# Kernel optimization log

Hardware: AMD Instinct MI355X
Metric: run time of the kernel (lower is better)

## Reference

```python
import jax, jax.numpy as jnp
import numpy as np
from jax import lax

B, N = 8, 4096
H = 128          # cfg.net.num_hidden
K = 64           # max_num_neighbors
R1, R2 = 0.2, 0.4
S1, S2 = N // 2, N // 8   # sampling ratios 0.5 and 0.25
OUT = 40


def setup_inputs() -> dict:
    key = jax.random.key(0)
    ks = jax.random.split(key, 32)
    inp = {}
    inp["x"] = jax.random.normal(ks[30], (B, N, 3), jnp.float32)
    inp["pos"] = jax.random.uniform(ks[31], (B, N, 3), jnp.float32)  # unit cube -> radii 0.2/0.4 meaningful
    layers = [("sa1_w1", "sa1_b1", 6, H // 2), ("sa1_w2", "sa1_b2", H // 2, H),
              ("sa2_w1", "sa2_b1", H + 3, H), ("sa2_w2", "sa2_b2", H, 2 * H),
              ("sa3_w1", "sa3_b1", 2 * H + 3, 2 * H), ("sa3_w2", "sa3_b2", 2 * H, 4 * H),
              ("sa3_w3", "sa3_b3", 4 * H, 8 * H),
              ("hd_w1", "hd_b1", 8 * H, 4 * H), ("hd_w2", "hd_b2", 4 * H, 2 * H),
              ("hd_w3", "hd_b3", 2 * H, OUT)]
    for i, (wn, bn, fi, fo) in enumerate(layers):
        inp[wn] = jax.random.normal(ks[i], (fi, fo), jnp.float32) / np.sqrt(fi)
        inp[bn] = jnp.zeros((fo,), jnp.float32)
    return inp


def _mlp(h, layers):
    # Linear+ReLU stack, plain last layer (PyG MLP plain_last=True, eval-mode BN is identity)
    n = len(layers)
    for i, (w, b) in enumerate(layers):
        h = h @ w + b
        if i < n - 1:
            h = jax.nn.relu(h)
    return h


def _fps(p, n_samples):
    # farthest point sampling on one cloud p: [N,3] -> [n_samples] int32
    Np = p.shape[0]

    def step(carry, _):
        min_d, last = carry
        d = jnp.sum((p - p[last]) ** 2, -1)
        min_d = jnp.minimum(min_d, d)
        return (min_d, jnp.argmax(min_d).astype(jnp.int32)), last

    _, idxs = lax.scan(step, (jnp.full((Np,), jnp.inf, p.dtype), jnp.int32(0)),
                       None, length=n_samples)
    return idxs


def _sa(xc, pc, n_samples, r, layers):
    # one SA layer on one cloud: xc [N,C], pc [N,3]
    idx = _fps(pc, n_samples)
    c = pc[idx]                                            # [S,3] centers
    d2 = jnp.sum((c[:, None, :] - pc[None, :, :]) ** 2, -1)  # [S,N]
    d2 = jnp.where(d2 <= r * r, d2, jnp.inf)               # ball query mask
    negd, nbr = lax.top_k(-d2, K)                          # K nearest inside ball
    valid = jnp.isfinite(negd)                             # [S,K]
    feat = jnp.concatenate([xc[nbr], pc[nbr] - c[:, None, :]], -1)  # [S,K,C+3]
    h = _mlp(feat, layers)                                 # [S,K,Cout]
    h = jnp.where(valid[..., None], h, -jnp.inf)
    return jnp.max(h, axis=1), c                           # max-pool over neighborhood


def reference(x, pos, sa1_w1, sa1_b1, sa1_w2, sa1_b2,
              sa2_w1, sa2_b1, sa2_w2, sa2_b2,
              sa3_w1, sa3_b1, sa3_w2, sa3_b2, sa3_w3, sa3_b3,
              hd_w1, hd_b1, hd_w2, hd_b2, hd_w3, hd_b3):
    x1, p1 = jax.vmap(lambda xc, pc: _sa(xc, pc, S1, R1,
                                         [(sa1_w1, sa1_b1), (sa1_w2, sa1_b2)]))(x, pos)
    x2, p2 = jax.vmap(lambda xc, pc: _sa(xc, pc, S2, R2,
                                         [(sa2_w1, sa2_b1), (sa2_w2, sa2_b2)]))(x1, p1)
    # GlobalSAModule: MLP(cat([x,pos])) then global max pool over remaining points
    g = _mlp(jnp.concatenate([x2, p2], -1),
             [(sa3_w1, sa3_b1), (sa3_w2, sa3_b2), (sa3_w3, sa3_b3)])
    g = jnp.max(g, axis=1)                                 # [B, 8H]
    # head MLP (dropout inactive at eval)
    return _mlp(g, [(hd_w1, hd_b1), (hd_w2, hd_b2), (hd_w3, hd_b3)])
```

## Files before the change

kernel.cpp:

```cpp
#include <hip/hip_runtime.h>


constexpr int NBATCH = 8;

template<int CTRL>
__device__ __forceinline__ float dpp_max_step(float v) {
  int o = __builtin_amdgcn_update_dpp(__float_as_int(v), __float_as_int(v),
                                      CTRL, 0xf, 0xf, false);
  return fmaxf(v, __int_as_float(o));
}
__device__ __forceinline__ float wave_max_bcast(float v) {
  v = dpp_max_step<0x111>(v);
  v = dpp_max_step<0x112>(v);
  v = dpp_max_step<0x114>(v);
  v = dpp_max_step<0x118>(v);
  v = dpp_max_step<0x142>(v);
  v = dpp_max_step<0x143>(v);
  return __int_as_float(__builtin_amdgcn_readlane(__float_as_int(v), 63));
}
template<int CTRL>
__device__ __forceinline__ int dpp_add_step(int v) {
  int o = __builtin_amdgcn_update_dpp(0, v, CTRL, 0xf, 0xf, true);
  return v + o;
}
__device__ __forceinline__ int wave_sum_bcast(int v) {
  v = dpp_add_step<0x111>(v);
  v = dpp_add_step<0x112>(v);
  v = dpp_add_step<0x114>(v);
  v = dpp_add_step<0x118>(v);
  v = dpp_add_step<0x142>(v);
  v = dpp_add_step<0x143>(v);
  return __builtin_amdgcn_readlane(v, 63);
}

__device__ void fps1_one(const float* __restrict__ p, float* __restrict__ cb) {
#pragma clang fp contract(off)
  constexpr int NTH = 256, PT = 16, NW = 4, NSAMP = 2048;
  __shared__ unsigned long long skey[2][NW];
  __shared__ float sxyz[2][NW][3];
  __shared__ float scb[NSAMP * 3];
  const int t = threadIdx.x, lane = t & 63, w = t >> 6;
  const float INF = __builtin_inff();
  float px[PT], py[PT], pz[PT], md[PT];
#pragma unroll
  for (int i = 0; i < PT; i++) {
    int j = t * PT + i;
    px[i] = p[j * 3 + 0]; py[i] = p[j * 3 + 1]; pz[i] = p[j * 3 + 2];
    md[i] = INF;
  }
  float cx = p[0], cy = p[1], cz = p[2];
  if (t == 0) { scb[0] = cx; scb[1] = cy; scb[2] = cz; }
  for (int s = 0; s < NSAMP - 1; ++s) {
#pragma unroll
    for (int i = 0; i < PT; i++) {
      float dx = px[i] - cx, dy = py[i] - cy, dz = pz[i] - cz;
      float d = (dx * dx + dy * dy) + dz * dz;
      md[i] = fminf(md[i], d);
    }
    float m8[8];
#pragma unroll
    for (int i = 0; i < 8; i++) m8[i] = fmaxf(md[i], md[i + 8]);
    float m4[4];
#pragma unroll
    for (int i = 0; i < 4; i++) m4[i] = fmaxf(m8[i], m8[i + 4]);
    float bv = fmaxf(fmaxf(m4[0], m4[1]), fmaxf(m4[2], m4[3]));
    int bi = 0;
#pragma unroll
    for (int i = PT - 1; i >= 1; --i) if (md[i] == bv) bi = i;
    float wmax = wave_max_bcast(bv);
    unsigned long long ball = __ballot(bv == wmax);
    int fl = __ffsll((long long)ball) - 1;
    int ib = __builtin_amdgcn_readlane(bi, fl);
    int gidx = ((w << 6) + fl) * PT + ib;
    float sx = px[0], sy = py[0], sz = pz[0];
#pragma unroll
    for (int k = 1; k < PT; k++)
      if (ib == k) { sx = px[k]; sy = py[k]; sz = pz[k]; }
    sx = __int_as_float(__builtin_amdgcn_readlane(__float_as_int(sx), fl));
    sy = __int_as_float(__builtin_amdgcn_readlane(__float_as_int(sy), fl));
    sz = __int_as_float(__builtin_amdgcn_readlane(__float_as_int(sz), fl));
    if (lane == 0) {
      skey[s & 1][w] = (((unsigned long long)(unsigned)__float_as_int(wmax)) << 32)
                       | (unsigned)(~gidx);
      sxyz[s & 1][w][0] = sx; sxyz[s & 1][w][1] = sy; sxyz[s & 1][w][2] = sz;
    }
    __syncthreads();
    unsigned long long best = skey[s & 1][0];
    float nx = sxyz[s & 1][0][0], ny = sxyz[s & 1][0][1], nz = sxyz[s & 1][0][2];
#pragma unroll
    for (int q = 1; q < NW; q++) {
      unsigned long long k2 = skey[s & 1][q];
      bool gt = k2 > best;
      best = gt ? k2 : best;
      nx = gt ? sxyz[s & 1][q][0] : nx;
      ny = gt ? sxyz[s & 1][q][1] : ny;
      nz = gt ? sxyz[s & 1][q][2] : nz;
    }
    cx = nx; cy = ny; cz = nz;
    if (t == 0) { scb[(s + 1) * 3 + 0] = cx; scb[(s + 1) * 3 + 1] = cy;
                  scb[(s + 1) * 3 + 2] = cz; }
  }
  __syncthreads();
  for (int i = t; i < NSAMP * 3; i += NTH) cb[i] = scb[i];
}

__device__ void fps2_one(const float* __restrict__ p, float* __restrict__ cb) {
#pragma clang fp contract(off)
  constexpr int NTH = 256, PT = 8, NW = 4, NSAMP = 512;
  __shared__ unsigned long long skey2[2][NW];
  __shared__ float sxyz2[2][NW][3];
  __shared__ float scb2[NSAMP * 3];
  const int t = threadIdx.x, lane = t & 63, w = t >> 6;
  const float INF = __builtin_inff();
  float px[PT], py[PT], pz[PT], md[PT];
#pragma unroll
  for (int i = 0; i < PT; i++) {
    int j = t * PT + i;
    px[i] = p[j * 3 + 0]; py[i] = p[j * 3 + 1]; pz[i] = p[j * 3 + 2];
    md[i] = INF;
  }
  float cx = p[0], cy = p[1], cz = p[2];
  if (t == 0) { scb2[0] = cx; scb2[1] = cy; scb2[2] = cz; }
  for (int s = 0; s < NSAMP - 1; ++s) {
#pragma unroll
    for (int i = 0; i < PT; i++) {
      float dx = px[i] - cx, dy = py[i] - cy, dz = pz[i] - cz;
      float d = (dx * dx + dy * dy) + dz * dz;
      md[i] = fminf(md[i], d);
    }
    float m4[4];
#pragma unroll
    for (int i = 0; i < 4; i++) m4[i] = fmaxf(md[i], md[i + 4]);
    float bv = fmaxf(fmaxf(m4[0], m4[1]), fmaxf(m4[2], m4[3]));
    int bi = 0;
#pragma unroll
    for (int i = PT - 1; i >= 1; --i) if (md[i] == bv) bi = i;
    float wmax = wave_max_bcast(bv);
    unsigned long long ball = __ballot(bv == wmax);
    int fl = __ffsll((long long)ball) - 1;
    int ib = __builtin_amdgcn_readlane(bi, fl);
    int gidx = ((w << 6) + fl) * PT + ib;
    float sx = px[0], sy = py[0], sz = pz[0];
#pragma unroll
    for (int k = 1; k < PT; k++)
      if (ib == k) { sx = px[k]; sy = py[k]; sz = pz[k]; }
    sx = __int_as_float(__builtin_amdgcn_readlane(__float_as_int(sx), fl));
    sy = __int_as_float(__builtin_amdgcn_readlane(__float_as_int(sy), fl));
    sz = __int_as_float(__builtin_amdgcn_readlane(__float_as_int(sz), fl));
    if (lane == 0) {
      skey2[s & 1][w] = (((unsigned long long)(unsigned)__float_as_int(wmax)) << 32)
                        | (unsigned)(~gidx);
      sxyz2[s & 1][w][0] = sx; sxyz2[s & 1][w][1] = sy; sxyz2[s & 1][w][2] = sz;
    }
    __syncthreads();
    unsigned long long best = skey2[s & 1][0];
    float nx = sxyz2[s & 1][0][0], ny = sxyz2[s & 1][0][1], nz = sxyz2[s & 1][0][2];
#pragma unroll
    for (int q = 1; q < NW; q++) {
      unsigned long long k2 = skey2[s & 1][q];
      bool gt = k2 > best;
      best = gt ? k2 : best;
      nx = gt ? sxyz2[s & 1][q][0] : nx;
      ny = gt ? sxyz2[s & 1][q][1] : ny;
      nz = gt ? sxyz2[s & 1][q][2] : nz;
    }
    cx = nx; cy = ny; cz = nz;
    if (t == 0) { scb2[(s + 1) * 3 + 0] = cx; scb2[(s + 1) * 3 + 1] = cy;
                  scb2[(s + 1) * 3 + 2] = cz; }
  }
  __syncthreads();
  for (int i = t; i < NSAMP * 3; i += NTH) cb[i] = scb2[i];
}

template<int NPTS, int SPB, int LCAP, int WPB>
__device__ void ballquery_body(int bb, const float* __restrict__ pts,
    const float* __restrict__ ctr, float rr,
    int* __restrict__ nbr, int* __restrict__ cnt_out) {
#pragma clang fp contract(off)
  constexpr int KREG = LCAP / 64;
  const int gw = bb * WPB + (threadIdx.x >> 6);
  const int lane = threadIdx.x & 63;
  const int b = gw / SPB;
  __shared__ unsigned long long list_[WPB][LCAP];
  unsigned long long* list = list_[threadIdx.x >> 6];
  const float* p = pts + (size_t)b * NPTS * 3;
  const float* c = ctr + (size_t)gw * 3;
  const float cx = c[0], cy = c[1], cz = c[2];
  const unsigned long long lmask = (1ull << lane) - 1ull;
  int cnt = 0;
  for (int j0 = 0; j0 < NPTS; j0 += 64) {
    int j = j0 + lane;
    float dx = p[j * 3 + 0] - cx, dy = p[j * 3 + 1] - cy, dz = p[j * 3 + 2] - cz;
    float d = (dx * dx + dy * dy) + dz * dz;
    bool in = (d <= rr);
    unsigned long long bal = __ballot(in);
    int pos = cnt + __popcll(bal & lmask);
    if (in && pos < LCAP)
      list[pos] = (((unsigned long long)__float_as_uint(d)) << 32) | (unsigned)j;
    cnt += __popcll(bal);
  }
  if (cnt > LCAP) cnt = LCAP;
  __syncthreads();
  int* nbrp = nbr + (size_t)gw * 64;
  const int nr = (cnt + 63) >> 6;
  unsigned long long key[KREG];
#pragma unroll
  for (int r = 0; r < KREG; r++) {
    int slot = r * 64 + lane;
    key[r] = (r < nr && slot < cnt) ? list[slot] : ~0ull;
  }
  if (cnt <= 64) {
    nbrp[lane] = (lane < cnt) ? (int)(unsigned)key[0] : 0;
    if (lane == 0) cnt_out[gw] = cnt;
    return;
  }
  unsigned pref = 0; int cbase = 0;
  for (int bit = 29; bit >= 0; --bit) {
    int cc = 0;
#pragma unroll
    for (int r = 0; r < KREG; r++) if (r < nr) {
      unsigned db = (unsigned)(key[r] >> 32);
      cc += ((db >> bit) == (pref >> bit)) ? 1 : 0;
    }
    cc = wave_sum_bcast(cc);
    if (cbase + cc < 64) { cbase += cc; pref |= (1u << bit); }
  }
  int base = 0;
#pragma unroll
  for (int r = 0; r < KREG; r++) if (r < nr) {
    unsigned db = (unsigned)(key[r] >> 32);
    bool sel = db < pref;
    unsigned long long m = __ballot(sel);
    if (sel) nbrp[base + __popcll(m & lmask)] = (int)(unsigned)key[r];
    base += __popcll(m);
  }
  int need = 64 - base;
  for (int t2 = 0; t2 < need; ++t2) {
    unsigned besti = 0xffffffffu;
#pragma unroll
    for (int r = 0; r < KREG; r++) if (r < nr) {
      if ((unsigned)(key[r] >> 32) == pref) {
        unsigned v = (unsigned)key[r];
        besti = v < besti ? v : besti;
      }
    }
#pragma unroll
    for (int off = 32; off; off >>= 1) {
      unsigned o = __shfl_xor(besti, off, 64);
      besti = o < besti ? o : besti;
    }
    unsigned long long wk = (((unsigned long long)pref) << 32) | besti;
#pragma unroll
    for (int r = 0; r < KREG; r++) if (r < nr && key[r] == wk) key[r] = ~0ull;
    if (lane == 0) nbrp[base + t2] = (int)besti;
  }
  if (lane == 0) cnt_out[gw] = 64;
}

__device__ void q1_body(int bb, const float* __restrict__ x,
    const float* __restrict__ pos, const float* __restrict__ w, float* __restrict__ q) {
  int gw = (bb << 2) + (threadIdx.x >> 6), lane = threadIdx.x & 63;
  const float* xr = x + (size_t)gw * 3; const float* pr = pos + (size_t)gw * 3;
  float a = 0.f;
#pragma unroll
  for (int m = 0; m < 3; m++) a = fmaf(xr[m], w[m * 64 + lane], a);
#pragma unroll
  for (int m = 0; m < 3; m++) a = fmaf(pr[m], w[(3 + m) * 64 + lane], a);
  q[(size_t)gw * 64 + lane] = a;
}

__device__ void t1_body(int bb, const float* __restrict__ c1,
    const float* __restrict__ w, const float* __restrict__ b1, float* __restrict__ t) {
  int gw = (bb << 2) + (threadIdx.x >> 6), lane = threadIdx.x & 63;
  const float* cr = c1 + (size_t)gw * 3;
  float a = b1[lane];
#pragma unroll
  for (int m = 0; m < 3; m++) a = fmaf(-cr[m], w[(3 + m) * 64 + lane], a);
  t[(size_t)gw * 64 + lane] = a;
}

__device__ void t2_body(int bb, const float* __restrict__ c2,
    const float* __restrict__ w, const float* __restrict__ b1, float* __restrict__ t) {
  int gw = (bb << 2) + (threadIdx.x >> 6), lane = threadIdx.x & 63;
  const float* cr = c2 + (size_t)gw * 3;
  float a0 = b1[lane], a1 = b1[64 + lane];
#pragma unroll
  for (int m = 0; m < 3; m++) {
    a0 = fmaf(-cr[m], w[(128 + m) * 128 + lane], a0);
    a1 = fmaf(-cr[m], w[(128 + m) * 128 + 64 + lane], a1);
  }
  t[(size_t)gw * 128 + lane] = a0;
  t[(size_t)gw * 128 + 64 + lane] = a1;
}

__device__ void concat3_body(int bb, const float* __restrict__ c2, float* __restrict__ xin3) {
  int row = bb * 256 + threadIdx.x;
  if (row < NBATCH * 512) {
    float* o = xin3 + (size_t)row * 272 + 256;
    const float* c = c2 + (size_t)row * 3;
    o[0] = c[0]; o[1] = c[1]; o[2] = c[2];
#pragma unroll
    for (int i = 3; i < 16; i++) o[i] = 0.f;
  }
}

template<int CIN, int COUT, int OSTR, int NPB, int SPB>
__device__ void sa_pool_body(int bb, const float* __restrict__ q,
    const float* __restrict__ t, const int* __restrict__ nbr, const int* __restrict__ cnt,
    const float* __restrict__ w2, const float* __restrict__ b2, float* __restrict__ out) {
  int gw = (bb << 2) + (threadIdx.x >> 6), lane = threadIdx.x & 63;
  int b = gw / SPB;
  int nk = nbr[(size_t)gw * 64 + lane];
  int c = cnt[gw];
  const float* qr = q + ((size_t)b * NPB + nk) * CIN;
  const float* tr = t + (size_t)gw * CIN;
  float h[CIN];
#pragma unroll
  for (int i = 0; i < CIN; i += 4) {
    float4 v = *(const float4*)(qr + i);
    h[i]     = fmaxf(v.x + tr[i], 0.f);
    h[i + 1] = fmaxf(v.y + tr[i + 1], 0.f);
    h[i + 2] = fmaxf(v.z + tr[i + 2], 0.f);
    h[i + 3] = fmaxf(v.w + tr[i + 3], 0.f);
  }
  bool valid = lane < c;
  float* op = out + (size_t)gw * OSTR;
#pragma unroll 1
  for (int nc = 0; nc < COUT; nc += 16) {
    float acc[16];
#pragma unroll
    for (int u = 0; u < 16; u++) acc[u] = b2[nc + u];
#pragma unroll
    for (int i = 0; i < CIN; i++) {
      const float* wr = w2 + (size_t)i * COUT + nc;
#pragma unroll
      for (int u = 0; u < 16; u++) acc[u] = fmaf(h[i], wr[u], acc[u]);
    }
#pragma unroll
    for (int u = 0; u < 16; u++) {
      float v = valid ? acc[u] : -__builtin_inff();
#pragma unroll
      for (int off = 32; off; off >>= 1) v = fmaxf(v, __shfl_xor(v, off, 64));
      acc[u] = v;
    }
    if (lane == 0) {
#pragma unroll
      for (int u = 0; u < 16; u += 4)
        *(float4*)(op + nc + u) = make_float4(acc[u], acc[u + 1], acc[u + 2], acc[u + 3]);
    }
  }
}

__global__ __attribute__((amdgpu_flat_work_group_size(256, 256),
                          amdgpu_waves_per_eu(1, 2)))
void fuse1_kernel(const float* __restrict__ pos,
    const float* __restrict__ x, const float* __restrict__ w11,
    float* __restrict__ c1, float* __restrict__ q1) {
  int bid = blockIdx.x;
  if (bid < 8)
    fps1_one(pos + (size_t)bid * 4096 * 3, c1 + (size_t)bid * 2048 * 3);
  else
    q1_body(bid - 8, x, pos, w11, q1);
}

__global__ __attribute__((amdgpu_flat_work_group_size(256, 256),
                          amdgpu_waves_per_eu(1, 2)))
void fuse2_kernel(const float* __restrict__ pos,
    const float* __restrict__ c1, const float* __restrict__ w11, const float* __restrict__ b11,
    float* __restrict__ c2, int* __restrict__ nbr1, int* __restrict__ cnt1,
    float* __restrict__ t1buf, float rr1) {
  int bid = blockIdx.x;
  if (bid < 8)
    fps2_one(c1 + (size_t)bid * 2048 * 3, c2 + (size_t)bid * 512 * 3);
  else if (bid < 8 + 4096)
    ballquery_body<4096, 2048, 512, 4>(bid - 8, pos, c1, rr1, nbr1, cnt1);
  else
    t1_body(bid - (8 + 4096), c1, w11, b11, t1buf);
}

__global__ __launch_bounds__(256) void fuse3_kernel(const float* __restrict__ q1buf,
    const float* __restrict__ t1buf, const int* __restrict__ nbr1, const int* __restrict__ cnt1,
    const float* __restrict__ w12, const float* __restrict__ b12, float* __restrict__ x1,
    const float* __restrict__ c1, const float* __restrict__ c2, float rr2,
    int* __restrict__ nbr2, int* __restrict__ cnt2,
    const float* __restrict__ w21, const float* __restrict__ b21, float* __restrict__ t2buf,
    float* __restrict__ xin3) {
  int bid = blockIdx.x;
  if (bid < 4096)
    sa_pool_body<64, 128, 128, 4096, 2048>(bid, q1buf, t1buf, nbr1, cnt1, w12, b12, x1);
  else if (bid < 4096 + 1024)
    ballquery_body<2048, 512, 1024, 4>(bid - 4096, c1, c2, rr2, nbr2, cnt2);
  else if (bid < 4096 + 1024 + 1024)
    t2_body(bid - (4096 + 1024), c2, w21, b21, t2buf);
  else
    concat3_body(bid - (4096 + 1024 + 1024), c2, xin3);
}

__global__ __launch_bounds__(256) void q2_kernel(const float* __restrict__ x1,
    const float* __restrict__ p1, const float* __restrict__ w, float* __restrict__ q2) {
  int gw = (blockIdx.x << 2) + (threadIdx.x >> 6), lane = threadIdx.x & 63;
  const float* xr = x1 + (size_t)gw * 128; const float* pr = p1 + (size_t)gw * 3;
  float a0 = 0.f, a1 = 0.f;
#pragma unroll 8
  for (int m = 0; m < 128; m++) {
    float v = xr[m];
    a0 = fmaf(v, w[m * 128 + lane], a0);
    a1 = fmaf(v, w[m * 128 + 64 + lane], a1);
  }
#pragma unroll
  for (int m = 0; m < 3; m++) {
    float v = pr[m];
    a0 = fmaf(v, w[(128 + m) * 128 + lane], a0);
    a1 = fmaf(v, w[(128 + m) * 128 + 64 + lane], a1);
  }
  q2[(size_t)gw * 128 + lane] = a0;
  q2[(size_t)gw * 128 + 64 + lane] = a1;
}

__global__ __launch_bounds__(256) void sa_pool2_kernel(const float* __restrict__ q,
    const float* __restrict__ t, const int* __restrict__ nbr, const int* __restrict__ cnt,
    const float* __restrict__ w2, const float* __restrict__ b2, float* __restrict__ out) {
  sa_pool_body<128, 256, 272, 2048, 512>(blockIdx.x, q, t, nbr, cnt, w2, b2, out);
}

template<int K, int KP, int N, int AST, bool RELU>
__global__ __launch_bounds__(256) void gemm64(const float* __restrict__ A,
    const float* __restrict__ W, const float* __restrict__ bias, float* __restrict__ C) {
  constexpr int NT = N / 64;
  const int bid = blockIdx.x, tid = threadIdx.x;
  const int tm = bid / NT, tn = bid % NT;
  __shared__ __align__(16) float As[16][68];
  __shared__ __align__(16) float Ws[16][68];
  const int arow = tid >> 2, acol = (tid & 3) << 2;
  const int wrow = tid >> 4, wcol = (tid & 15) << 2;
  const int ty = tid >> 4, tx = tid & 15;
  const float* Ap = A + (size_t)(tm * 64 + arow) * AST + acol;
  const float* Wp = W + (size_t)tn * 64 + wcol;
  float acc[4][4] = {};
  for (int k0 = 0; k0 < KP; k0 += 16) {
    float4 av = *(const float4*)(Ap + k0);
    As[acol + 0][arow] = av.x; As[acol + 1][arow] = av.y;
    As[acol + 2][arow] = av.z; As[acol + 3][arow] = av.w;
    int krow = k0 + wrow;
    float4 wv = make_float4(0.f, 0.f, 0.f, 0.f);
    if (krow < K) wv = *(const float4*)(Wp + (size_t)krow * N);
    *(float4*)(&Ws[wrow][wcol]) = wv;
    __syncthreads();
#pragma unroll
    for (int kk = 0; kk < 16; kk++) {
      float4 a4 = *(const float4*)(&As[kk][ty << 2]);
      float4 b4 = *(const float4*)(&Ws[kk][tx << 2]);
      float aa[4] = {a4.x, a4.y, a4.z, a4.w};
      float bb[4] = {b4.x, b4.y, b4.z, b4.w};
#pragma unroll
      for (int mm = 0; mm < 4; mm++)
#pragma unroll
        for (int nn = 0; nn < 4; nn++) acc[mm][nn] = fmaf(aa[mm], bb[nn], acc[mm][nn]);
    }
    __syncthreads();
  }
  const int m0 = tm * 64 + (ty << 2), n0 = tn * 64 + (tx << 2);
#pragma unroll
  for (int mm = 0; mm < 4; mm++) {
    float4 o;
    o.x = acc[mm][0] + bias[n0 + 0];
    o.y = acc[mm][1] + bias[n0 + 1];
    o.z = acc[mm][2] + bias[n0 + 2];
    o.w = acc[mm][3] + bias[n0 + 3];
    if (RELU) { o.x = fmaxf(o.x, 0.f); o.y = fmaxf(o.y, 0.f);
                o.z = fmaxf(o.z, 0.f); o.w = fmaxf(o.w, 0.f); }
    *(float4*)(C + (size_t)(m0 + mm) * N + n0) = o;
  }
}

__global__ void gmax_kernel(const float* __restrict__ h, float* __restrict__ g) {
  int n = blockIdx.x * 256 + threadIdx.x;
  int b = n >> 10, col = n & 1023;
  const float* p = h + ((size_t)b * 512) * 1024 + col;
  float m = -__builtin_inff();
  for (int j = 0; j < 512; j++) m = fmaxf(m, p[(size_t)j * 1024]);
  g[n] = m;
}

__global__ __launch_bounds__(256) void head_kernel(const float* __restrict__ g,
    const float* __restrict__ w1, const float* __restrict__ b1,
    const float* __restrict__ w2, const float* __restrict__ b2,
    const float* __restrict__ w3, const float* __restrict__ b3,
    float* __restrict__ out) {
  int b = blockIdx.x, t = threadIdx.x;
  __shared__ float s1[1024];
  __shared__ float s2[512];
  *(float4*)(s1 + t * 4) = *(const float4*)(g + (size_t)b * 1024 + t * 4);
  __syncthreads();
  {
    float a0 = b1[t], a1 = b1[t + 256];
    for (int i = 0; i < 1024; i++) {
      float v = s1[i];
      a0 = fmaf(v, w1[(size_t)i * 512 + t], a0);
      a1 = fmaf(v, w1[(size_t)i * 512 + t + 256], a1);
    }
    s2[t] = fmaxf(a0, 0.f); s2[t + 256] = fmaxf(a1, 0.f);
  }
  __syncthreads();
  {
    float a = b2[t];
    for (int i = 0; i < 512; i++) a = fmaf(s2[i], w2[(size_t)i * 256 + t], a);
    s1[t] = fmaxf(a, 0.f);
  }
  __syncthreads();
  if (t < 40) {
    float a = b3[t];
    for (int i = 0; i < 256; i++) a = fmaf(s1[i], w3[(size_t)i * 40 + t], a);
    out[(size_t)b * 40 + t] = a;
  }
}

extern "C" void kernel_launch(void* const* d_in, const int* in_sizes, int n_in,
                              void* d_out, int out_size, void* d_ws, size_t ws_size,
                              hipStream_t stream) {
  const float* x   = (const float*)d_in[0];
  const float* pos = (const float*)d_in[1];
  const float* w11 = (const float*)d_in[2];  const float* b11 = (const float*)d_in[3];
  const float* w12 = (const float*)d_in[4];  const float* b12 = (const float*)d_in[5];
  const float* w21 = (const float*)d_in[6];  const float* b21 = (const float*)d_in[7];
  const float* w22 = (const float*)d_in[8];  const float* b22 = (const float*)d_in[9];
  const float* w31 = (const float*)d_in[10]; const float* b31 = (const float*)d_in[11];
  const float* w32 = (const float*)d_in[12]; const float* b32 = (const float*)d_in[13];
  const float* w33 = (const float*)d_in[14]; const float* b33 = (const float*)d_in[15];
  const float* hw1 = (const float*)d_in[16]; const float* hb1 = (const float*)d_in[17];
  const float* hw2 = (const float*)d_in[18]; const float* hb2 = (const float*)d_in[19];
  const float* hw3 = (const float*)d_in[20]; const float* hb3 = (const float*)d_in[21];
  float* out = (float*)d_out;

  char* wsb = (char*)d_ws;
  int*   cnt1 = (int*)(wsb + 81920);
  int*   cnt2 = (int*)(wsb + 147456);
  float* c1   = (float*)(wsb + 163840);
  float* c2   = (float*)(wsb + 360448);
  float* g    = (float*)(wsb + 409600);
  char* big = wsb + 524288;
  int*   nbr1 = (int*)(big + 0);
  float* q1   = (float*)(big + 4194304);
  float* t1   = (float*)(big + 12582912);
  float* h3c  = (float*)(big + 0);
  float* x1   = (float*)(big + 16777216);
  int*   nbr2 = (int*)(big + 25165824);
  float* h3b  = (float*)(big + 16777216);
  float* q2   = (float*)(big + 26214400);
  float* h3a  = (float*)(big + 26214400);
  float* t2   = (float*)(big + 34603008);
  float* xin3 = (float*)(big + 36700160);

  const float RR1 = (float)(0.2 * 0.2);
  const float RR2 = (float)(0.4 * 0.4);

  fuse1_kernel<<<8 + 8192, 256, 0, stream>>>(pos, x, w11, c1, q1);
  fuse2_kernel<<<8 + 4096 + 4096, 256, 0, stream>>>(pos, c1, w11, b11,
                                                    c2, nbr1, cnt1, t1, RR1);
  fuse3_kernel<<<4096 + 1024 + 1024 + 16, 256, 0, stream>>>(q1, t1, nbr1, cnt1,
      w12, b12, x1, c1, c2, RR2, nbr2, cnt2, w21, b21, t2, xin3);
  q2_kernel<<<4096, 256, 0, stream>>>(x1, c1, w21, q2);
  sa_pool2_kernel<<<1024, 256, 0, stream>>>(q2, t2, nbr2, cnt2, w22, b22, xin3);
  gemm64<259, 272, 256, 272, true ><<<256,  256, 0, stream>>>(xin3, w31, b31, h3a);
  gemm64<256, 256, 512, 256, true ><<<512,  256, 0, stream>>>(h3a,  w32, b32, h3b);
  gemm64<512, 512, 1024, 512, false><<<1024, 256, 0, stream>>>(h3b, w33, b33, h3c);
  gmax_kernel<<<32, 256, 0, stream>>>(h3c, g);
  head_kernel<<<NBATCH, 256, 0, stream>>>(g, hw1, hb1, hw2, hb2, hw3, hb3, out);

  (void)in_sizes; (void)n_in; (void)out_size; (void)ws_size;
}
```

Baseline: 3.616 ms.

## Reschedule fused stages so FPS2 overlaps SA1 pooling instead of ball query

```diff
diff --git a/kernel.cpp b/kernel.cpp
--- a/kernel.cpp
+++ b/kernel.cpp
@@ -293,6 +293,27 @@
   t[(size_t)gw * 128 + 64 + lane] = a1;
 }
 
+__device__ void q2_body(int bb, const float* __restrict__ x1,
+    const float* __restrict__ p1, const float* __restrict__ w, float* __restrict__ q2) {
+  int gw = (bb << 2) + (threadIdx.x >> 6), lane = threadIdx.x & 63;
+  const float* xr = x1 + (size_t)gw * 128; const float* pr = p1 + (size_t)gw * 3;
+  float a0 = 0.f, a1 = 0.f;
+#pragma unroll 8
+  for (int m = 0; m < 128; m++) {
+    float v = xr[m];
+    a0 = fmaf(v, w[m * 128 + lane], a0);
+    a1 = fmaf(v, w[m * 128 + 64 + lane], a1);
+  }
+#pragma unroll
+  for (int m = 0; m < 3; m++) {
+    float v = pr[m];
+    a0 = fmaf(v, w[(128 + m) * 128 + lane], a0);
+    a1 = fmaf(v, w[(128 + m) * 128 + 64 + lane], a1);
+  }
+  q2[(size_t)gw * 128 + lane] = a0;
+  q2[(size_t)gw * 128 + 64 + lane] = a1;
+}
+
 __device__ void concat3_body(int bb, const float* __restrict__ c2, float* __restrict__ xin3) {
   int row = bb * 256 + threadIdx.x;
   if (row < NBATCH * 512) {
@@ -363,58 +384,42 @@
     q1_body(bid - 8, x, pos, w11, q1);
 }
 
-__global__ __attribute__((amdgpu_flat_work_group_size(256, 256),
-                          amdgpu_waves_per_eu(1, 2)))
-void fuse2_kernel(const float* __restrict__ pos,
+__global__ __launch_bounds__(256) void stage2_kernel(const float* __restrict__ pos,
     const float* __restrict__ c1, const float* __restrict__ w11, const float* __restrict__ b11,
-    float* __restrict__ c2, int* __restrict__ nbr1, int* __restrict__ cnt1,
-    float* __restrict__ t1buf, float rr1) {
+    int* __restrict__ nbr1, int* __restrict__ cnt1, float* __restrict__ t1buf, float rr1) {
+  int bid = blockIdx.x;
+  if (bid < 4096)
+    ballquery_body<4096, 2048, 512, 4>(bid, pos, c1, rr1, nbr1, cnt1);
+  else
+    t1_body(bid - 4096, c1, w11, b11, t1buf);
+}
+
+__global__ __launch_bounds__(256) void stage3_kernel(const float* __restrict__ c1,
+    float* __restrict__ c2,
+    const float* __restrict__ q1buf, const float* __restrict__ t1buf,
+    const int* __restrict__ nbr1, const int* __restrict__ cnt1,
+    const float* __restrict__ w12, const float* __restrict__ b12, float* __restrict__ x1) {
   int bid = blockIdx.x;
   if (bid < 8)
     fps2_one(c1 + (size_t)bid * 2048 * 3, c2 + (size_t)bid * 512 * 3);
-  else if (bid < 8 + 4096)
-    ballquery_body<4096, 2048, 512, 4>(bid - 8, pos, c1, rr1, nbr1, cnt1);
   else
-    t1_body(bid - (8 + 4096), c1, w11, b11, t1buf);
-}
-
-__global__ __launch_bounds__(256) void fuse3_kernel(const float* __restrict__ q1buf,
-    const float* __restrict__ t1buf, const int* __restrict__ nbr1, const int* __restrict__ cnt1,
-    const float* __restrict__ w12, const float* __restrict__ b12, float* __restrict__ x1,
-    const float* __restrict__ c1, const float* __restrict__ c2, float rr2,
+    sa_pool_body<64, 128, 128, 4096, 2048>(bid - 8, q1buf, t1buf, nbr1, cnt1, w12, b12, x1);
+}
+
+__global__ __launch_bounds__(256) void stage4_kernel(const float* __restrict__ c1,
+    const float* __restrict__ c2, float rr2,
     int* __restrict__ nbr2, int* __restrict__ cnt2,
     const float* __restrict__ w21, const float* __restrict__ b21, float* __restrict__ t2buf,
-    float* __restrict__ xin3) {
+    const float* __restrict__ x1, float* __restrict__ q2buf, float* __restrict__ xin3) {
   int bid = blockIdx.x;
-  if (bid < 4096)
-    sa_pool_body<64, 128, 128, 4096, 2048>(bid, q1buf, t1buf, nbr1, cnt1, w12, b12, x1);
-  else if (bid < 4096 + 1024)
-    ballquery_body<2048, 512, 1024, 4>(bid - 4096, c1, c2, rr2, nbr2, cnt2);
-  else if (bid < 4096 + 1024 + 1024)
-    t2_body(bid - (4096 + 1024), c2, w21, b21, t2buf);
+  if (bid < 1024)
+    ballquery_body<2048, 512, 1024, 4>(bid, c1, c2, rr2, nbr2, cnt2);
+  else if (bid < 1024 + 1024)
+    t2_body(bid - 1024, c2, w21, b21, t2buf);
+  else if (bid < 1024 + 1024 + 4096)
+    q2_body(bid - 2048, x1, c1, w21, q2buf);
   else
-    concat3_body(bid - (4096 + 1024 + 1024), c2, xin3);
-}
-
-__global__ __launch_bounds__(256) void q2_kernel(const float* __restrict__ x1,
-    const float* __restrict__ p1, const float* __restrict__ w, float* __restrict__ q2) {
-  int gw = (blockIdx.x << 2) + (threadIdx.x >> 6), lane = threadIdx.x & 63;
-  const float* xr = x1 + (size_t)gw * 128; const float* pr = p1 + (size_t)gw * 3;
-  float a0 = 0.f, a1 = 0.f;
-#pragma unroll 8
-  for (int m = 0; m < 128; m++) {
-    float v = xr[m];
-    a0 = fmaf(v, w[m * 128 + lane], a0);
-    a1 = fmaf(v, w[m * 128 + 64 + lane], a1);
-  }
-#pragma unroll
-  for (int m = 0; m < 3; m++) {
-    float v = pr[m];
-    a0 = fmaf(v, w[(128 + m) * 128 + lane], a0);
-    a1 = fmaf(v, w[(128 + m) * 128 + 64 + lane], a1);
-  }
-  q2[(size_t)gw * 128 + lane] = a0;
-  q2[(size_t)gw * 128 + 64 + lane] = a1;
+    concat3_body(bid - (1024 + 1024 + 4096), c2, xin3);
 }
 
 __global__ __launch_bounds__(256) void sa_pool2_kernel(const float* __restrict__ q,
@@ -555,11 +560,12 @@
   const float RR2 = (float)(0.4 * 0.4);
 
   fuse1_kernel<<<8 + 8192, 256, 0, stream>>>(pos, x, w11, c1, q1);
-  fuse2_kernel<<<8 + 4096 + 4096, 256, 0, stream>>>(pos, c1, w11, b11,
-                                                    c2, nbr1, cnt1, t1, RR1);
-  fuse3_kernel<<<4096 + 1024 + 1024 + 16, 256, 0, stream>>>(q1, t1, nbr1, cnt1,
-      w12, b12, x1, c1, c2, RR2, nbr2, cnt2, w21, b21, t2, xin3);
-  q2_kernel<<<4096, 256, 0, stream>>>(x1, c1, w21, q2);
+  stage2_kernel<<<4096 + 4096, 256, 0, stream>>>(pos, c1, w11, b11,
+                                                 nbr1, cnt1, t1, RR1);
+  stage3_kernel<<<8 + 4096, 256, 0, stream>>>(c1, c2, q1, t1, nbr1, cnt1,
+                                              w12, b12, x1);
+  stage4_kernel<<<1024 + 1024 + 4096 + 16, 256, 0, stream>>>(c1, c2, RR2,
+      nbr2, cnt2, w21, b21, t2, x1, q2, xin3);
   sa_pool2_kernel<<<1024, 256, 0, stream>>>(q2, t2, nbr2, cnt2, w22, b22, xin3);
   gemm64<259, 272, 256, 272, true ><<<256,  256, 0, stream>>>(xin3, w31, b31, h3a);
   gemm64<256, 256, 512, 256, true ><<<512,  256, 0, stream>>>(h3a,  w32, b32, h3b);
```

Result: faster. 3.419 ms (-5.4%).
